# Performance work log

Hardware: AMD Instinct MI355X
Metric: run time of the kernel (lower is better)

## Reference

```python
import jax, jax.numpy as jnp
import numpy as np
import math

N_HEADS = 8

def setup_inputs() -> dict:
    key = jax.random.key(0)
    ks = jax.random.split(key, 5)
    B, S, D = 2, 2048, 512
    return {
        "x": jax.random.normal(ks[0], (B, S, D), dtype=jnp.float32),
        "w_in": jax.random.normal(ks[1], (3 * D, D), dtype=jnp.float32) * (1.0 / math.sqrt(D)),
        "b_in": jax.random.normal(ks[2], (3 * D,), dtype=jnp.float32) * 0.01,
        "w_out": jax.random.normal(ks[3], (D, D), dtype=jnp.float32) * (1.0 / math.sqrt(D)),
        "b_out": jax.random.normal(ks[4], (D,), dtype=jnp.float32) * 0.01,
        "casual_mask": 1,
    }

def reference(x, w_in, b_in, w_out, b_out, casual_mask):
    B, S, D = x.shape
    H = N_HEADS
    dh = D // H
    # in_proj: torch Linear -> x @ W.T + b
    qvk = x @ w_in.T + b_in  # [B, S, 3D]
    # NOTE: source unpacks as q, v, k (chunk order quirk preserved)
    q, v, k = jnp.split(qvk, 3, axis=-1)
    # [B, S, D] -> [B, H, S, dh]
    def to_heads(t):
        return t.reshape(B, S, H, dh).transpose(0, 2, 1, 3)
    q, k, v = to_heads(q), to_heads(k), to_heads(v)
    scores = jnp.einsum("bhqd,bhkd->bhqk", q, k)  # [B, H, S, S]
    if casual_mask:
        # mask BEFORE scaling, as in the source (-inf unaffected by division)
        tri = jnp.triu(jnp.ones((S, S), dtype=bool), k=1)
        scores = jnp.where(tri, -jnp.inf, scores)
    scores = scores / math.sqrt(dh)
    attn = jax.nn.softmax(scores, axis=-1)
    out = jnp.einsum("bhqk,bhkd->bhqd", attn, v)  # [B, H, S, dh]
    out = out.transpose(0, 2, 1, 3).reshape(B, S, D)
    return out @ w_out.T + b_out
```

## Files before the change

kernel.cpp:

```cpp
#include <hip/hip_runtime.h>
#include <hip/hip_bf16.h>

typedef unsigned short u16;
typedef unsigned int u32;
typedef __attribute__((ext_vector_type(8))) short bf16x8;
typedef __attribute__((ext_vector_type(4))) short bf16x4;
typedef __attribute__((ext_vector_type(4))) float f32x4;

#define DEVI __device__ __forceinline__

DEVI u16 f2bf(float f) {
  union { float f; unsigned int u; } v; v.f = f;
  unsigned int u = v.u;
  unsigned int r = (u + 0x7fffu + ((u >> 16) & 1u)) >> 16;
  return (u16)r;
}

DEVI float bf2f(u16 b) {
  union { unsigned int u; float f; } v; v.u = ((unsigned int)b) << 16;
  return v.f;
}

DEVI float fexp2(float x) {
#if __has_builtin(__builtin_amdgcn_exp2f)
  return __builtin_amdgcn_exp2f(x);
#else
  return exp2f(x);
#endif
}

DEVI u32 pkbf(float a, float b) {
  union { float f; u32 u; } ua, ub;
  ua.f = a; ub.f = b;
  return __builtin_amdgcn_perm(ua.u + 0x8000u, ub.u + 0x8000u, 0x07060302u);
}

DEVI void lds_cp16(u16* lds, const u16* g) {
  __builtin_amdgcn_global_load_lds(
      (const __attribute__((address_space(1))) u32*)g,
      (__attribute__((address_space(3))) u32*)lds, 16, 0, 0);
}

DEVI f32x4 mfma16x16x16_bf16(bf16x4 a, bf16x4 b, f32x4 c) {
#if __has_builtin(__builtin_amdgcn_mfma_f32_16x16x16bf16_1k)
  return __builtin_amdgcn_mfma_f32_16x16x16bf16_1k(a, b, c, 0, 0, 0);
#else
  f32x4 d;
  asm volatile("v_mfma_f32_16x16x16_bf16 %0, %1, %2, %3"
               : "=v"(d) : "v"(a), "v"(b), "v"(c));
  return d;
#endif
}

__global__ __launch_bounds__(256) void cvt_all(
    const float4* __restrict__ x, const float4* __restrict__ wi,
    const float4* __restrict__ wo, u16* __restrict__ xb,
    u16* __restrict__ wib, u16* __restrict__ wob) {
  int i = blockIdx.x * 256 + threadIdx.x;
  const float4* src; u16* dst; int off;
  if (i < 524288)      { src = x;  dst = xb;  off = i; }
  else if (i < 720896) { src = wi; dst = wib; off = i - 524288; }
  else                 { src = wo; dst = wob; off = i - 720896; }
  float4 f = src[off];
  ushort4 o;
  o.x = f2bf(f.x); o.y = f2bf(f.y); o.z = f2bf(f.z); o.w = f2bf(f.w);
  ((ushort4*)dst)[off] = o;
}

__global__ __launch_bounds__(256) void inproj_gemm(
    const u16* __restrict__ xb, const u16* __restrict__ wb,
    const float* __restrict__ bin,
    u16* __restrict__ Qb, u16* __restrict__ Kb, u16* __restrict__ Vt) {
  const int K = 512;
  const float SCL = 0.180336878f;
  __shared__ u16 SMEM[16384];
  u16 (*At)[4096] = (u16 (*)[4096])(SMEM);
  u16 (*Bt)[4096] = (u16 (*)[4096])(SMEM + 8192);
  int tid = threadIdx.x;
  int w = tid >> 6, lane = tid & 63;
  int ql = lane & 15, quad = lane >> 4;
  int wr = w >> 1, wc = w & 1;
  int mtile = blockIdx.x * 128, ntile = blockIdx.y * 128;

  int r4 = lane >> 2, c4 = lane & 3;
  int swz4 = c4 ^ (r4 & 3);

  const u16* ag0 = xb + (size_t)(mtile + w * 32 + r4) * K + swz4 * 8;
  const u16* bg0 = wb + (size_t)(ntile + w * 32 + r4) * K + swz4 * 8;

  f32x4 acc[4][4];
#pragma unroll
  for (int t = 0; t < 4; ++t)
#pragma unroll
    for (int u = 0; u < 4; ++u) acc[t][u] = (f32x4){0, 0, 0, 0};

  lds_cp16(&At[0][w * 1024], ag0);
  lds_cp16(&At[0][w * 1024 + 512], ag0 + 16 * K);
  lds_cp16(&Bt[0][w * 1024], bg0);
  lds_cp16(&Bt[0][w * 1024 + 512], bg0 + 16 * K);

  int cb = ql & 3;
  for (int kk = 0; kk < 16; ++kk) {
    int cur = kk & 1;
    __syncthreads();
    if (kk < 15) {
      int k0 = (kk + 1) * 32;
      lds_cp16(&At[cur ^ 1][w * 1024], ag0 + k0);
      lds_cp16(&At[cur ^ 1][w * 1024 + 512], ag0 + 16 * K + k0);
      lds_cp16(&Bt[cur ^ 1][w * 1024], bg0 + k0);
      lds_cp16(&Bt[cur ^ 1][w * 1024 + 512], bg0 + 16 * K + k0);
    }
    bf16x8 af[4], bf[4];
#pragma unroll
    for (int t = 0; t < 4; ++t) {
      int row = wr * 64 + t * 16 + ql;
      af[t] = *(const bf16x8*)(&At[cur][row * 32 + ((quad ^ cb) * 8)]);
    }
#pragma unroll
    for (int u = 0; u < 4; ++u) {
      int row = wc * 64 + u * 16 + ql;
      bf[u] = *(const bf16x8*)(&Bt[cur][row * 32 + ((quad ^ cb) * 8)]);
    }
#pragma unroll
    for (int t = 0; t < 4; ++t)
#pragma unroll
      for (int u = 0; u < 4; ++u)
        acc[t][u] = __builtin_amdgcn_mfma_f32_16x16x32_bf16(af[t], bf[u], acc[t][u], 0, 0, 0);
  }

  if (blockIdx.y >= 4 && blockIdx.y < 8) {
    __syncthreads();
    u16* T = SMEM;
#pragma unroll
    for (int u = 0; u < 4; ++u) {
      int d_local = wc * 64 + u * 16 + ql;
      float bias = bin[ntile + d_local];
#pragma unroll
      for (int t = 0; t < 4; ++t) {
        int s_local = wr * 64 + t * 16 + quad * 4;
        union { ushort4 v; u16 e[4]; } pk;
#pragma unroll
        for (int r = 0; r < 4; ++r) pk.e[r] = f2bf(acc[t][u][r] + bias);
        int ch = s_local >> 3;
        int sw = ch ^ (d_local & 15);
        *(ushort4*)(&T[d_local * 128 + sw * 8 + (s_local & 7)]) = pk.v;
      }
    }
    __syncthreads();
    int h0 = (ntile - 512) >> 6;
    int b = mtile >> 11;
    int smb = mtile & 2047;
    int s8 = lane & 15;
#pragma unroll
    for (int i = 0; i < 8; ++i) {
      int d_local = i * 16 + w * 4 + (lane >> 4);
      int sw = s8 ^ (d_local & 15);
      bf16x8 vrow = *(const bf16x8*)(&T[d_local * 128 + sw * 8]);
      int h = h0 + (d_local >> 6);
      int dh = d_local & 63;
      *(bf16x8*)(&Vt[(((size_t)(b * 8 + h)) * 64 + dh) * 2048 + smb + s8 * 8]) = vrow;
    }
  } else {
    int chunk = (int)(blockIdx.y >> 2);
#pragma unroll
    for (int u = 0; u < 4; ++u) {
      int n = ntile + wc * 64 + u * 16 + ql;
      float bias = bin[n];
      int nc = n & 511;
      int h = nc >> 6, d = nc & 63;
#pragma unroll
      for (int t = 0; t < 4; ++t)
#pragma unroll
        for (int r = 0; r < 4; ++r) {
          int m = mtile + wr * 64 + t * 16 + quad * 4 + r;
          int b = m >> 11, s = m & 2047;
          float v = acc[t][u][r] + bias;
          size_t idx = (((size_t)(b * 8 + h)) * 2048 + s) * 64 + d;
          if (chunk == 0) Qb[idx] = f2bf(v * SCL);
          else            Kb[idx] = f2bf(v);
        }
    }
  }
}

__global__ __launch_bounds__(256) void attn_kernel(
    const u16* __restrict__ Qb, const u16* __restrict__ Kb,
    const u16* __restrict__ Vt, u16* __restrict__ Pp, float* __restrict__ Ml) {
  const int S = 2048;
  __shared__ u16 Kt[2][4096];
  __shared__ u16 Vl[2][4096];
  int tid = threadIdx.x;
  int w = tid >> 6, lane = tid & 63;
  int ql = lane & 15, quad = lane >> 4;
  int j = blockIdx.x;
  int c = blockIdx.y;
  int bh = blockIdx.z;
  int tileA = j, tileB = 31 - j;
  int qbaseA = tileA * 64 + w * 16;
  int qbaseB = tileB * 64 + w * 16;
  const u16* Qh = Qb + (size_t)bh * S * 64;
  const u16* Kh = Kb + (size_t)bh * S * 64;
  const u16* Vh = Vt + (size_t)bh * 64 * S;

  int r8 = lane >> 3, c8 = lane & 7;
  int swz = c8 ^ r8;
  int cb = ql & 7;

  bf16x8 qA0 = *(const bf16x8*)(Qh + (size_t)(qbaseA + ql) * 64 + quad * 8);
  bf16x8 qA1 = *(const bf16x8*)(Qh + (size_t)(qbaseA + ql) * 64 + 32 + quad * 8);
  bf16x8 qB0 = *(const bf16x8*)(Qh + (size_t)(qbaseB + ql) * 64 + quad * 8);
  bf16x8 qB1 = *(const bf16x8*)(Qh + (size_t)(qbaseB + ql) * 64 + 32 + quad * 8);

  f32x4 oA[4] = {{0,0,0,0},{0,0,0,0},{0,0,0,0},{0,0,0,0}};
  f32x4 oB[4] = {{0,0,0,0},{0,0,0,0},{0,0,0,0},{0,0,0,0}};
  float lA = 0.0f, lB = 0.0f;

  auto kbOf = [&](int i) { return (i <= j) ? i : (i - j - 1); };
  auto stage = [&](int buf, int kbase) {
    const u16* kg = Kh + (size_t)(kbase + w * 16 + r8) * 64 + swz * 8;
    lds_cp16(&Kt[buf][w * 1024], kg);
    lds_cp16(&Kt[buf][w * 1024 + 512], kg + 8 * 64);
    const u16* vg = Vh + (size_t)(w * 16 + r8) * S + kbase + swz * 8;
    lds_cp16(&Vl[buf][w * 1024], vg);
    lds_cp16(&Vl[buf][w * 1024 + 512], vg + 8 * S);
  };
  auto process = [&](int cur, int kbase, int qbase, bf16x8 x0, bf16x8 x1,
                     f32x4 (&o)[4], float& l) {
    int q = qbase + ql;
    f32x4 st[4];
#pragma unroll
    for (int t = 0; t < 4; ++t) {
      const u16* kr = &Kt[cur][(t * 16 + ql) * 64];
      bf16x8 kf0 = *(const bf16x8*)(kr + ((quad ^ cb) * 8));
      bf16x8 kf1 = *(const bf16x8*)(kr + (((quad + 4) ^ cb) * 8));
      f32x4 s = {0, 0, 0, 0};
      s = __builtin_amdgcn_mfma_f32_16x16x32_bf16(kf0, x0, s, 0, 0, 0);
      s = __builtin_amdgcn_mfma_f32_16x16x32_bf16(kf1, x1, s, 0, 0, 0);
      st[t] = s;
    }
    bool needmask = (kbase + 63 > qbase);
    float e[4][4];
#pragma unroll
    for (int t = 0; t < 4; ++t)
#pragma unroll
      for (int r = 0; r < 4; ++r) {
        float v = st[t][r];
        if (needmask) {
          int key = kbase + t * 16 + quad * 4 + r;
          if (key > q) v = -3.0e38f;
        }
        e[t][r] = fexp2(v);
      }
    float s0 = (e[0][0] + e[0][1]) + (e[0][2] + e[0][3]);
    float s1 = (e[1][0] + e[1][1]) + (e[1][2] + e[1][3]);
    float s2 = (e[2][0] + e[2][1]) + (e[2][2] + e[2][3]);
    float s3 = (e[3][0] + e[3][1]) + (e[3][2] + e[3][3]);
    l += (s0 + s1) + (s2 + s3);
    bf16x4 p[4];
#pragma unroll
    for (int t = 0; t < 4; ++t) {
      union { bf16x4 v; u32 u[2]; } pk;
      pk.u[0] = pkbf(e[t][1], e[t][0]);
      pk.u[1] = pkbf(e[t][3], e[t][2]);
      p[t] = pk.v;
    }
#pragma unroll
    for (int t = 0; t < 4; ++t)
#pragma unroll
      for (int d = 0; d < 4; ++d) {
        const u16* vr = &Vl[cur][(d * 16 + ql) * 64];
        bf16x4 vf = *(const bf16x4*)(vr + (((t * 2 + (quad >> 1)) ^ cb) * 8 + (quad & 1) * 4));
        o[d] = mfma16x16x16_bf16(vf, p[t], o[d]);
      }
  };

  stage(0, kbOf(c * 11) * 64);

  for (int r = 0; r < 11; ++r) {
    int i = c * 11 + r;
    int cur = r & 1;
    __syncthreads();
    if (r < 10) stage(cur ^ 1, kbOf(i + 1) * 64);
    if (i <= j) process(cur, i * 64, qbaseA, qA0, qA1, oA, lA);
    else        process(cur, (i - j - 1) * 64, qbaseB, qB0, qB1, oB, lB);
  }

  lA += __shfl_xor(lA, 16); lA += __shfl_xor(lA, 32);
  lB += __shfl_xor(lB, 16); lB += __shfl_xor(lB, 32);
  int qrow = w * 16 + ql;
  size_t pb = ((((size_t)c * 16 + bh) * 16 + j) * 2) * 4096;
  size_t mb = ((((size_t)c * 16 + bh) * 16 + j) * 2) * 64;
  if (quad == 0) {
    Ml[mb + qrow]      = lA;
    Ml[mb + 64 + qrow] = lB;
  }
  bool validA = (c * 11 <= j);
  bool validB = (c * 11 + 10 > j);
  if (validA) {
#pragma unroll
    for (int dt = 0; dt < 4; ++dt) {
      ushort4 v;
      v.x = f2bf(oA[dt][0]); v.y = f2bf(oA[dt][1]);
      v.z = f2bf(oA[dt][2]); v.w = f2bf(oA[dt][3]);
      *(ushort4*)(Pp + pb + qrow * 64 + dt * 16 + quad * 4) = v;
    }
  }
  if (validB) {
#pragma unroll
    for (int dt = 0; dt < 4; ++dt) {
      ushort4 v;
      v.x = f2bf(oB[dt][0]); v.y = f2bf(oB[dt][1]);
      v.z = f2bf(oB[dt][2]); v.w = f2bf(oB[dt][3]);
      *(ushort4*)(Pp + pb + 4096 + qrow * 64 + dt * 16 + quad * 4) = v;
    }
  }
}

__global__ __launch_bounds__(256) void attn_merge(
    const u16* __restrict__ Pp, const float* __restrict__ Ml,
    u16* __restrict__ Ob) {
  int tid = threadIdx.x;
  int j = blockIdx.x, t = blockIdx.y, bh = blockIdx.z;
  int q = tid >> 2, ds = (tid & 3) * 16;
  float lc[3], L = 0.0f;
#pragma unroll
  for (int c = 0; c < 3; ++c) {
    lc[c] = Ml[((((size_t)c * 16 + bh) * 16 + j) * 2 + t) * 64 + q];
    L += lc[c];
  }
  float O[16];
#pragma unroll
  for (int i = 0; i < 16; ++i) O[i] = 0.0f;
#pragma unroll
  for (int c = 0; c < 3; ++c) {
    if (lc[c] > 0.0f) {
      size_t pb = ((((size_t)c * 16 + bh) * 16 + j) * 2 + t) * 4096 + q * 64 + ds;
      union { bf16x8 v; u16 e[8]; } a, b;
      a.v = *(const bf16x8*)(Pp + pb);
      b.v = *(const bf16x8*)(Pp + pb + 8);
#pragma unroll
      for (int i = 0; i < 8; ++i) {
        O[i]     += bf2f(a.e[i]);
        O[i + 8] += bf2f(b.e[i]);
      }
    }
  }
  float inv = 1.0f / L;
  int tile_abs = t ? (31 - j) : j;
  int s = tile_abs * 64 + q;
  int b2 = bh >> 3, h = bh & 7;
  size_t row = ((size_t)(b2 * 2048 + s)) * 512 + h * 64 + ds;
  union { bf16x8 v; u16 e[8]; } o0, o1;
#pragma unroll
  for (int i = 0; i < 8; ++i) {
    o0.e[i] = f2bf(O[i] * inv);
    o1.e[i] = f2bf(O[i + 8] * inv);
  }
  *(bf16x8*)(Ob + row)     = o0.v;
  *(bf16x8*)(Ob + row + 8) = o1.v;
}

__global__ __launch_bounds__(256) void outproj_gemm(
    const u16* __restrict__ Ob, const u16* __restrict__ wb,
    const float* __restrict__ bout, float* __restrict__ out) {
  const int K = 512;
  __shared__ u16 At[2][64 * 32];
  __shared__ u16 Bt[2][128 * 32];
  int tid = threadIdx.x;
  int w = tid >> 6, lane = tid & 63;
  int ql = lane & 15, quad = lane >> 4;
  int wr = w >> 1, wc = w & 1;
  int mtile = blockIdx.x * 64, ntile = blockIdx.y * 128;

  int r4 = lane >> 2, c4 = lane & 3;
  int swz4 = c4 ^ (r4 & 3);

  const u16* ag0 = Ob + (size_t)(mtile + w * 16 + r4) * K + swz4 * 8;
  const u16* bg0 = wb + (size_t)(ntile + w * 32 + r4) * K + swz4 * 8;

  f32x4 acc[2][4];
#pragma unroll
  for (int t = 0; t < 2; ++t)
#pragma unroll
    for (int u = 0; u < 4; ++u) acc[t][u] = (f32x4){0, 0, 0, 0};

  lds_cp16(&At[0][w * 512], ag0);
  lds_cp16(&Bt[0][w * 1024], bg0);
  lds_cp16(&Bt[0][w * 1024 + 512], bg0 + 16 * K);

  int cb = ql & 3;
  for (int kk = 0; kk < 16; ++kk) {
    int cur = kk & 1;
    __syncthreads();
    if (kk < 15) {
      int k0 = (kk + 1) * 32;
      lds_cp16(&At[cur ^ 1][w * 512], ag0 + k0);
      lds_cp16(&Bt[cur ^ 1][w * 1024], bg0 + k0);
      lds_cp16(&Bt[cur ^ 1][w * 1024 + 512], bg0 + 16 * K + k0);
    }
    bf16x8 af[2], bf[4];
#pragma unroll
    for (int t = 0; t < 2; ++t) {
      int row = wr * 32 + t * 16 + ql;
      af[t] = *(const bf16x8*)(&At[cur][row * 32 + ((quad ^ cb) * 8)]);
    }
#pragma unroll
    for (int u = 0; u < 4; ++u) {
      int row = wc * 64 + u * 16 + ql;
      bf[u] = *(const bf16x8*)(&Bt[cur][row * 32 + ((quad ^ cb) * 8)]);
    }
#pragma unroll
    for (int t = 0; t < 2; ++t)
#pragma unroll
      for (int u = 0; u < 4; ++u)
        acc[t][u] = __builtin_amdgcn_mfma_f32_16x16x32_bf16(af[t], bf[u], acc[t][u], 0, 0, 0);
  }

#pragma unroll
  for (int u = 0; u < 4; ++u) {
    int n = ntile + wc * 64 + u * 16 + ql;
    float bias = bout[n];
#pragma unroll
    for (int t = 0; t < 2; ++t)
#pragma unroll
      for (int r = 0; r < 4; ++r) {
        int mm = mtile + wr * 32 + t * 16 + quad * 4 + r;
        out[(size_t)mm * 512 + n] = acc[t][u][r] + bias;
      }
  }
}

extern "C" void kernel_launch(void* const* d_in, const int* in_sizes, int n_in,
                              void* d_out, int out_size, void* d_ws, size_t ws_size,
                              hipStream_t stream) {
  const float* x     = (const float*)d_in[0];
  const float* w_in  = (const float*)d_in[1];
  const float* b_in  = (const float*)d_in[2];
  const float* w_out = (const float*)d_in[3];
  const float* b_out = (const float*)d_in[4];
  float* out = (float*)d_out;
  char* ws = (char*)d_ws;

  u16* xb    = (u16*)(ws);
  u16* winb  = (u16*)(ws + 4194304);
  u16* woutb = (u16*)(ws + 5767168);
  u16* Qb    = (u16*)(ws + 6291456);
  u16* Kb    = (u16*)(ws + 10485760);
  u16* Vt    = (u16*)(ws + 14680064);
  u16* Ob    = (u16*)(ws + 18874368);
  u16* Pp    = (u16*)(ws + 23068672);
  float* Ml  = (float*)(ws + 35651584);

  cvt_all<<<3072, 256, 0, stream>>>((const float4*)x, (const float4*)w_in,
                                    (const float4*)w_out, xb, winb, woutb);
  inproj_gemm<<<dim3(32, 12), 256, 0, stream>>>(xb, winb, b_in, Qb, Kb, Vt);
  attn_kernel<<<dim3(16, 3, 16), 256, 0, stream>>>(Qb, Kb, Vt, Pp, Ml);
  attn_merge<<<dim3(16, 2, 16), 256, 0, stream>>>(Pp, Ml, Ob);
  outproj_gemm<<<dim3(64, 4), 256, 0, stream>>>(Ob, woutb, b_out, out);
}
```

Baseline: 125.0 us.

## Fuse split-KV attention merge into output projection GEMM A-tile staging

Removes the separate attn_merge kernel. The output projection GEMM now builds its A tile directly from the three partial attention outputs (Pp) and their row sums (Ml), normalizing them in registers and writing bf16 into LDS. This drops one kernel launch and the write and re-read of the Ob intermediate. In exchange, each of the 4 N-tile blocks recomputes the merge, so partial data is read four times, and the A staging becomes synchronous global loads plus arithmetic instead of async LDS copies.

```diff
diff --git a/kernel.cpp b/kernel.cpp
--- a/kernel.cpp
+++ b/kernel.cpp
@@ -316,53 +316,10 @@
   }
 }
 
-__global__ __launch_bounds__(256) void attn_merge(
+__global__ __launch_bounds__(256) void outproj_gemm(
     const u16* __restrict__ Pp, const float* __restrict__ Ml,
-    u16* __restrict__ Ob) {
-  int tid = threadIdx.x;
-  int j = blockIdx.x, t = blockIdx.y, bh = blockIdx.z;
-  int q = tid >> 2, ds = (tid & 3) * 16;
-  float lc[3], L = 0.0f;
-#pragma unroll
-  for (int c = 0; c < 3; ++c) {
-    lc[c] = Ml[((((size_t)c * 16 + bh) * 16 + j) * 2 + t) * 64 + q];
-    L += lc[c];
-  }
-  float O[16];
-#pragma unroll
-  for (int i = 0; i < 16; ++i) O[i] = 0.0f;
-#pragma unroll
-  for (int c = 0; c < 3; ++c) {
-    if (lc[c] > 0.0f) {
-      size_t pb = ((((size_t)c * 16 + bh) * 16 + j) * 2 + t) * 4096 + q * 64 + ds;
-      union { bf16x8 v; u16 e[8]; } a, b;
-      a.v = *(const bf16x8*)(Pp + pb);
-      b.v = *(const bf16x8*)(Pp + pb + 8);
-#pragma unroll
-      for (int i = 0; i < 8; ++i) {
-        O[i]     += bf2f(a.e[i]);
-        O[i + 8] += bf2f(b.e[i]);
-      }
-    }
-  }
-  float inv = 1.0f / L;
-  int tile_abs = t ? (31 - j) : j;
-  int s = tile_abs * 64 + q;
-  int b2 = bh >> 3, h = bh & 7;
-  size_t row = ((size_t)(b2 * 2048 + s)) * 512 + h * 64 + ds;
-  union { bf16x8 v; u16 e[8]; } o0, o1;
-#pragma unroll
-  for (int i = 0; i < 8; ++i) {
-    o0.e[i] = f2bf(O[i] * inv);
-    o1.e[i] = f2bf(O[i + 8] * inv);
-  }
-  *(bf16x8*)(Ob + row)     = o0.v;
-  *(bf16x8*)(Ob + row + 8) = o1.v;
-}
-
-__global__ __launch_bounds__(256) void outproj_gemm(
-    const u16* __restrict__ Ob, const u16* __restrict__ wb,
-    const float* __restrict__ bout, float* __restrict__ out) {
+    const u16* __restrict__ wb, const float* __restrict__ bout,
+    float* __restrict__ out) {
   const int K = 512;
   __shared__ u16 At[2][64 * 32];
   __shared__ u16 Bt[2][128 * 32];
@@ -375,16 +332,59 @@
   int r4 = lane >> 2, c4 = lane & 3;
   int swz4 = c4 ^ (r4 & 3);
 
-  const u16* ag0 = Ob + (size_t)(mtile + w * 16 + r4) * K + swz4 * 8;
+  int b = mtile >> 11;
+  int tile_abs = (mtile & 2047) >> 6;
+  int j   = (tile_abs < 16) ? tile_abs : 31 - tile_abs;
+  int t01 = (tile_abs < 16) ? 0 : 1;
+  bool v0, v1, v2;
+  if (t01 == 0) { v0 = true;     v1 = (j >= 11); v2 = (j >= 22); }
+  else          { v0 = (j < 10); v1 = (j < 21);  v2 = true;      }
+  int q = w * 16 + r4;
+  const size_t cP = (size_t)16 * 16 * 2 * 4096;
+  const size_t cM = (size_t)16 * 16 * 2 * 64;
+
   const u16* bg0 = wb + (size_t)(ntile + w * 32 + r4) * K + swz4 * 8;
 
+  auto stageA = [&](int buf, int kk) {
+    int h = kk >> 1;
+    size_t hb = ((size_t)(b * 8 + h) * 16 + j) * 2 + t01;
+    size_t pb = hb * 4096 + (size_t)q * 64 + (kk & 1) * 32 + swz4 * 8;
+    size_t mb = hb * 64 + q;
+    float L = Ml[mb] + Ml[mb + cM] + Ml[mb + 2 * cM];
+    float O[8];
+#pragma unroll
+    for (int i = 0; i < 8; ++i) O[i] = 0.0f;
+    if (v0) {
+      union { bf16x8 v; u16 e[8]; } a; a.v = *(const bf16x8*)(Pp + pb);
+#pragma unroll
+      for (int i = 0; i < 8; ++i) O[i] += bf2f(a.e[i]);
+    }
+    if (v1) {
+      union { bf16x8 v; u16 e[8]; } a; a.v = *(const bf16x8*)(Pp + pb + cP);
+#pragma unroll
+      for (int i = 0; i < 8; ++i) O[i] += bf2f(a.e[i]);
+    }
+    if (v2) {
+      union { bf16x8 v; u16 e[8]; } a; a.v = *(const bf16x8*)(Pp + pb + 2 * cP);
+#pragma unroll
+      for (int i = 0; i < 8; ++i) O[i] += bf2f(a.e[i]);
+    }
+    float inv = 1.0f / L;
+    union { bf16x8 v; u32 u[4]; } pk;
+    pk.u[0] = pkbf(O[1] * inv, O[0] * inv);
+    pk.u[1] = pkbf(O[3] * inv, O[2] * inv);
+    pk.u[2] = pkbf(O[5] * inv, O[4] * inv);
+    pk.u[3] = pkbf(O[7] * inv, O[6] * inv);
+    *(bf16x8*)(&At[buf][w * 512 + lane * 8]) = pk.v;
+  };
+
   f32x4 acc[2][4];
 #pragma unroll
   for (int t = 0; t < 2; ++t)
 #pragma unroll
     for (int u = 0; u < 4; ++u) acc[t][u] = (f32x4){0, 0, 0, 0};
 
-  lds_cp16(&At[0][w * 512], ag0);
+  stageA(0, 0);
   lds_cp16(&Bt[0][w * 1024], bg0);
   lds_cp16(&Bt[0][w * 1024 + 512], bg0 + 16 * K);
 
@@ -394,7 +394,7 @@
     __syncthreads();
     if (kk < 15) {
       int k0 = (kk + 1) * 32;
-      lds_cp16(&At[cur ^ 1][w * 512], ag0 + k0);
+      stageA(cur ^ 1, kk + 1);
       lds_cp16(&Bt[cur ^ 1][w * 1024], bg0 + k0);
       lds_cp16(&Bt[cur ^ 1][w * 1024 + 512], bg0 + 16 * K + k0);
     }
@@ -447,7 +447,6 @@
   u16* Qb    = (u16*)(ws + 6291456);
   u16* Kb    = (u16*)(ws + 10485760);
   u16* Vt    = (u16*)(ws + 14680064);
-  u16* Ob    = (u16*)(ws + 18874368);
   u16* Pp    = (u16*)(ws + 23068672);
   float* Ml  = (float*)(ws + 35651584);
 
@@ -455,6 +454,5 @@
                                     (const float4*)w_out, xb, winb, woutb);
   inproj_gemm<<<dim3(32, 12), 256, 0, stream>>>(xb, winb, b_in, Qb, Kb, Vt);
   attn_kernel<<<dim3(16, 3, 16), 256, 0, stream>>>(Qb, Kb, Vt, Pp, Ml);
-  attn_merge<<<dim3(16, 2, 16), 256, 0, stream>>>(Pp, Ml, Ob);
-  outproj_gemm<<<dim3(64, 4), 256, 0, stream>>>(Ob, woutb, b_out, out);
-}
+  outproj_gemm<<<dim3(64, 4), 256, 0, stream>>>(Pp, Ml, woutb, b_out, out);
+}
```

Result: slower. 130.1 us (+4.1%).
